# Optimization experiments

Hardware: AMD Instinct MI355X
Metric: run time of the kernel (lower is better)

## Reference

```python
import jax, jax.numpy as jnp
import numpy as np

SCALE = 4          # cfg['stride']
S = 7              # rcnn_crop_size
MAX_SIDE = 64      # max proposal side length in voxels (matches setup_inputs)
# max feature-space crop length = MAX_SIDE/SCALE + 2 (floor/ceil expansion) = 18
WMAX = int(np.ceil((MAX_SIDE // SCALE + 2) / S)) + 1  # = 4, adaptive-pool window bound


def setup_inputs() -> dict:
    key = jax.random.key(0)
    k1, k2, k3, k4 = jax.random.split(key, 4)
    B, C = 2, 128
    D, H, W = 128, 256, 256
    f = jax.random.normal(k1, (B, C, D // SCALE, H // SCALE, W // SCALE), jnp.float32)
    inputs = jnp.zeros((B, 1, D, H, W), jnp.float32)  # only shape is used by forward
    N = 32
    b = jax.random.randint(k2, (N,), 0, B).astype(jnp.float32)
    score = jnp.ones((N,), jnp.float32)
    cz = jax.random.uniform(k3, (N,), minval=32.0, maxval=float(D - 32))
    cy = jax.random.uniform(jax.random.fold_in(k3, 1), (N,), minval=32.0, maxval=float(H - 32))
    cx = jax.random.uniform(jax.random.fold_in(k3, 2), (N,), minval=32.0, maxval=float(W - 32))
    sides = jax.random.randint(k4, (N, 3), 16, MAX_SIDE + 1).astype(jnp.float32)
    proposals = jnp.stack([b, score, cz, cy, cx, sides[:, 0], sides[:, 1], sides[:, 2]], axis=1)
    return {"f": f, "inputs": inputs, "proposals": proposals}


def _crop_pool(f, b, c0, L, feat_dims):
    """Adaptive max-pool3d of f[b, :, c0:c0+L] to [C,S,S,S] via fixed-size masked windows."""
    i = jnp.arange(S)
    # torch adaptive pooling: start=floor(i*L/S), end=ceil((i+1)*L/S)
    start = (i[:, None] * L[None, :]) // S                       # [S,3]
    end = ((i[:, None] + 1) * L[None, :] + S - 1) // S           # [S,3]
    idx = c0[None, :, None] + start[:, :, None] + jnp.arange(WMAX)[None, None, :]  # [S,3,WMAX]
    valid = idx < (c0[None, :, None] + end[:, :, None])
    idx = jnp.minimum(idx, jnp.asarray(feat_dims, jnp.int32)[None, :, None] - 1)
    iz, iy, ix = idx[:, 0], idx[:, 1], idx[:, 2]                 # each [S,WMAX]
    vz, vy, vx = valid[:, 0], valid[:, 1], valid[:, 2]
    # gather [C, S, WMAX, S, WMAX, S, WMAX]
    g = f[b][:, iz[:, :, None, None, None, None],
             iy[None, None, :, :, None, None],
             ix[None, None, None, None, :, :]]
    m = (vz[:, :, None, None, None, None]
         & vy[None, None, :, :, None, None]
         & vx[None, None, None, None, :, :])
    g = jnp.where(m[None], g, -jnp.inf)
    return g.max(axis=(2, 4, 6))  # [C, S, S, S]


def reference(f, inputs, proposals):
    D, H, W = inputs.shape[2:]
    feat_dims = (D // SCALE, H // SCALE, W // SCALE)
    b = proposals[:, 0].astype(jnp.int32)
    center = proposals[:, 2:5]
    side = proposals[:, 5:8]
    c0 = jnp.floor((center - side / 2) / SCALE).astype(jnp.int32)
    c1 = jnp.ceil((center + side / 2) / SCALE).astype(jnp.int32)
    lim = jnp.asarray(feat_dims, jnp.int32)
    c0 = jnp.maximum(c0, 0)
    c1 = jnp.minimum(c1, lim[None, :])
    L = c1 - c0  # [N,3] crop lengths per axis
    pooled = jax.vmap(lambda bb, cc, ll: _crop_pool(f, bb, cc, ll, feat_dims))(b, c0, L)
    return pooled  # [N, C, S, S, S]
```

## Files before the change

kernel.cpp:

```cpp
#include <hip/hip_runtime.h>
#include <math.h>


constexpr int C_CH = 128;
constexpr int FD = 32, FH = 64, FW = 64;
constexpr int CH_VOL = FD * FH * FW;
constexpr int LMAX = 17;
constexpr int VOL = LMAX * LMAX * LMAX;
constexpr int CPB = 2;
constexpr int THREADS = 256;

__global__ __launch_bounds__(THREADS) void crop_roi_kernel(
    const float* __restrict__ f,
    const float* __restrict__ proposals,
    float* __restrict__ out)
{
    __shared__ float lds[CPB * VOL];

    const int n    = blockIdx.x;
    const int c0ch = blockIdx.y * CPB;

    const float* p = proposals + n * 8;
    const int   b  = (int)p[0];
    const float cz = p[2], cy = p[3], cx = p[4];
    const float sz = p[5], sy = p[6], sx = p[7];

    const int c0z = max((int)floorf((cz - sz * 0.5f) * 0.25f), 0);
    const int c0y = max((int)floorf((cy - sy * 0.5f) * 0.25f), 0);
    const int c0x = max((int)floorf((cx - sx * 0.5f) * 0.25f), 0);
    const int c1z = min((int)ceilf((cz + sz * 0.5f) * 0.25f), FD);
    const int c1y = min((int)ceilf((cy + sy * 0.5f) * 0.25f), FH);
    const int c1x = min((int)ceilf((cx + sx * 0.5f) * 0.25f), FW);
    const int Lz = c1z - c0z, Ly = c1y - c0y, Lx = c1x - c0x;

    const float* fb = f + (size_t)(b * C_CH + c0ch) * CH_VOL
                        + c0z * (FH * FW) + c0y * FW + c0x;
    #pragma unroll 4
    for (int e = threadIdx.x; e < CPB * VOL; e += THREADS) {
        int cl = e / VOL;
        int r  = e % VOL;
        int z  = r / (LMAX * LMAX);
        int y  = (r / LMAX) % LMAX;
        int x  = r % LMAX;
        int zc = min(z, Lz - 1);
        int yc = min(y, Ly - 1);
        int xc = min(x, Lx - 1);
        lds[e] = fb[(size_t)cl * CH_VOL + zc * (FH * FW) + yc * FW + xc];
    }
    __syncthreads();

    for (int o = threadIdx.x; o < CPB * 343; o += THREADS) {
        int cl = o / 343;
        int r  = o % 343;
        int iz = r / 49, iy = (r / 7) % 7, ix = r % 7;

        int zs = (iz * Lz) / 7, ze = ((iz + 1) * Lz + 6) / 7;
        int ys = (iy * Ly) / 7, ye = ((iy + 1) * Ly + 6) / 7;
        int xs = (ix * Lx) / 7, xe = ((ix + 1) * Lx + 6) / 7;

        const float* Lp = lds + cl * VOL;
        float m = -INFINITY;
        for (int z = zs; z < ze; ++z) {
            for (int y = ys; y < ye; ++y) {
                int base = z * (LMAX * LMAX) + y * LMAX;
                int xm = xe - 1;
                float v0 = Lp[base + xs];
                float v1 = Lp[base + min(xs + 1, xm)];
                float v2 = Lp[base + min(xs + 2, xm)];
                float v3 = Lp[base + min(xs + 3, xm)];
                m = fmaxf(m, fmaxf(fmaxf(v0, v1), fmaxf(v2, v3)));
            }
        }
        out[(size_t)(n * C_CH + c0ch) * 343 + o] = m;
    }
}

extern "C" void kernel_launch(void* const* d_in, const int* in_sizes, int n_in,
                              void* d_out, int out_size, void* d_ws, size_t ws_size,
                              hipStream_t stream) {
    const float* f         = (const float*)d_in[0];
    const float* proposals = (const float*)d_in[2];
    float* out             = (float*)d_out;

    dim3 grid(32, C_CH / CPB);
    crop_roi_kernel<<<grid, THREADS, 0, stream>>>(f, proposals, out);
}
```

Baseline: 217.8 us.

## Load only valid crop region with row-wise coalesced copies and share pooling bounds

The global-to-LDS copy now walks only the actual Lz×Ly×Lx crop, mapping lanes to x and warps to rows, instead of the padded 17^3 volume with clamped indices and per-element div/mod. Pooling window bounds are precomputed once per block in shared memory, and each thread now computes both channels for one output cell, reusing the index math. This cuts redundant global loads and integer arithmetic. The trade-off is that only 32 lanes per row are used (x-width up to 17), so half of each wavefront may idle during the copy.

```diff
diff --git a/kernel.cpp b/kernel.cpp
--- a/kernel.cpp
+++ b/kernel.cpp
@@ -16,6 +16,7 @@
     float* __restrict__ out)
 {
     __shared__ float lds[CPB * VOL];
+    __shared__ int ws_[3][7], we_[3][7];
 
     const int n    = blockIdx.x;
     const int c0ch = blockIdx.y * CPB;
@@ -33,45 +34,55 @@
     const int c1x = min((int)ceilf((cx + sx * 0.5f) * 0.25f), FW);
     const int Lz = c1z - c0z, Ly = c1y - c0y, Lx = c1x - c0x;
 
+    if (threadIdx.x < 21) {
+        const int d = threadIdx.x / 7;
+        const int i = threadIdx.x % 7;
+        const int L = (d == 0) ? Lz : (d == 1) ? Ly : Lx;
+        ws_[d][i] = (i * L) / 7;
+        we_[d][i] = ((i + 1) * L + 6) / 7;
+    }
+
+    const int tx = threadIdx.x & 31;
+    const int ty = threadIdx.x >> 5;
     const float* fb = f + (size_t)(b * C_CH + c0ch) * CH_VOL
                         + c0z * (FH * FW) + c0y * FW + c0x;
-    #pragma unroll 4
-    for (int e = threadIdx.x; e < CPB * VOL; e += THREADS) {
-        int cl = e / VOL;
-        int r  = e % VOL;
-        int z  = r / (LMAX * LMAX);
-        int y  = (r / LMAX) % LMAX;
-        int x  = r % LMAX;
-        int zc = min(z, Lz - 1);
-        int yc = min(y, Ly - 1);
-        int xc = min(x, Lx - 1);
-        lds[e] = fb[(size_t)cl * CH_VOL + zc * (FH * FW) + yc * FW + xc];
+    for (int cl = 0; cl < CPB; ++cl) {
+        const float* fc = fb + (size_t)cl * CH_VOL;
+        float* Lc = lds + cl * VOL;
+        if (tx < Lx) {
+            for (int z = 0; z < Lz; ++z) {
+                const float* fz = fc + z * (FH * FW);
+                float* Lzp = Lc + z * (LMAX * LMAX);
+                for (int y = ty; y < Ly; y += 8) {
+                    Lzp[y * LMAX + tx] = fz[y * FW + tx];
+                }
+            }
+        }
     }
     __syncthreads();
 
-    for (int o = threadIdx.x; o < CPB * 343; o += THREADS) {
-        int cl = o / 343;
-        int r  = o % 343;
-        int iz = r / 49, iy = (r / 7) % 7, ix = r % 7;
+    for (int r = threadIdx.x; r < 343; r += THREADS) {
+        const int iz = r / 49, iy = (r / 7) % 7, ix = r % 7;
+        const int zs = ws_[0][iz], ze = we_[0][iz];
+        const int ys = ws_[1][iy], ye = we_[1][iy];
+        const int xs = ws_[2][ix], xm = we_[2][ix] - 1;
+        const int x1 = min(xs + 1, xm);
+        const int x2 = min(xs + 2, xm);
+        const int x3 = min(xs + 3, xm);
 
-        int zs = (iz * Lz) / 7, ze = ((iz + 1) * Lz + 6) / 7;
-        int ys = (iy * Ly) / 7, ye = ((iy + 1) * Ly + 6) / 7;
-        int xs = (ix * Lx) / 7, xe = ((ix + 1) * Lx + 6) / 7;
-
-        const float* Lp = lds + cl * VOL;
-        float m = -INFINITY;
+        float m0 = -INFINITY, m1 = -INFINITY;
         for (int z = zs; z < ze; ++z) {
             for (int y = ys; y < ye; ++y) {
-                int base = z * (LMAX * LMAX) + y * LMAX;
-                int xm = xe - 1;
-                float v0 = Lp[base + xs];
-                float v1 = Lp[base + min(xs + 1, xm)];
-                float v2 = Lp[base + min(xs + 2, xm)];
-                float v3 = Lp[base + min(xs + 3, xm)];
-                m = fmaxf(m, fmaxf(fmaxf(v0, v1), fmaxf(v2, v3)));
+                const int base = z * (LMAX * LMAX) + y * LMAX;
+                const float* L0 = lds + base;
+                const float* L1 = lds + VOL + base;
+                m0 = fmaxf(m0, fmaxf(fmaxf(L0[xs], L0[x1]), fmaxf(L0[x2], L0[x3])));
+                m1 = fmaxf(m1, fmaxf(fmaxf(L1[xs], L1[x1]), fmaxf(L1[x2], L1[x3])));
             }
         }
-        out[(size_t)(n * C_CH + c0ch) * 343 + o] = m;
+        const size_t ob = (size_t)(n * C_CH + c0ch) * 343 + r;
+        out[ob]       = m0;
+        out[ob + 343] = m1;
     }
 }
 
```

Result: slower. 257.1 us (+18.1%).
